# Performance work log

Measured on AMD Instinct MI355X. Metric: run time of the kernel, lower is better.

The kernel has to match this reference:

```python
import jax, jax.numpy as jnp
import numpy as np

N_NODES = 100000
N_EDGES = 1600000
DIMS = [21, 32, 64, 128, 21]  # conv1..conv4 (conv4 in-dim fixed to 128; source's 100 is a bug)


def _glorot(key, fan_in, fan_out):
    s = jnp.sqrt(6.0 / (fan_in + fan_out))
    return jax.random.uniform(key, (fan_in, fan_out), jnp.float32, -s, s)


def setup_inputs() -> dict:
    key = jax.random.key(0)
    ks = jax.random.split(key, 6)
    x = jax.random.normal(ks[0], (N_NODES, DIMS[0]), jnp.float32)
    edge_index = jax.random.randint(ks[1], (2, N_EDGES), 0, N_NODES, jnp.int64)
    inp = {"x": x, "edge_index": edge_index}
    wkeys = jax.random.split(ks[2], 4)
    for i in range(4):
        inp[f"W{i+1}"] = _glorot(wkeys[i], DIMS[i], DIMS[i + 1])
        inp[f"b{i+1}"] = jnp.zeros((DIMS[i + 1],), jnp.float32)
    return inp


def gcn_conv(x, row, col, W, b):
    # PyG GCNConv: h = x W; symmetric normalization with self loops; aggregate; + bias
    N = x.shape[0]
    h = x @ W  # [N, F]
    deg = jnp.zeros((N,), h.dtype).at[col].add(1.0) + 1.0  # +1 for self loop
    dinv = jax.lax.rsqrt(deg)
    norm = dinv[row] * dinv[col]  # [E]
    agg = jnp.zeros_like(h).at[col].add(norm[:, None] * h[row])  # scatter messages
    agg = agg + (dinv * dinv)[:, None] * h  # self-loop contribution
    return agg + b


def reference(x, edge_index, W1, b1, W2, b2, W3, b3, W4, b4):
    row, col = edge_index[0], edge_index[1]
    x = jax.nn.relu(gcn_conv(x, row, col, W1, b1))
    x = jax.nn.relu(gcn_conv(x, row, col, W2, b2))
    x = jax.nn.relu(gcn_conv(x, row, col, W3, b3))
    x = gcn_conv(x, row, col, W4, b4)
    return x
```

## Files before the change

### kernel.cpp

```cpp
#include <hip/hip_runtime.h>

#define NN 100000
#define NE 1600000
#define SH 7
#define NB_BKT 782
#define BCAP 3072
#define CSRCAP 3200
#define CHUNK 8192

static inline int cdiv(long long a, int b) { return (int)((a + b - 1) / b); }

__global__ void partition_kernel(const int* __restrict__ row, const int* __restrict__ col,
                                 int* __restrict__ bcur,
                                 unsigned int* __restrict__ packed, int E) {
    __shared__ int lh[NB_BKT];
    __shared__ int lbase[NB_BKT];
    for (int i = threadIdx.x; i < NB_BKT; i += 256) lh[i] = 0;
    __syncthreads();
    int base = blockIdx.x * CHUNK;
    int end = min(base + CHUNK, E);
    for (int e = base + threadIdx.x; e < end; e += 256) atomicAdd(&lh[col[e] >> SH], 1);
    __syncthreads();
    for (int i = threadIdx.x; i < NB_BKT; i += 256) {
        int v = lh[i];
        lbase[i] = v ? atomicAdd(&bcur[i], v) : 0;
        lh[i] = 0;
    }
    __syncthreads();
    for (int e = base + threadIdx.x; e < end; e += 256) {
        int c = col[e];
        int r = row[e];
        int b = c >> SH;
        int off = atomicAdd(&lh[b], 1);
        packed[lbase[b] + off] = ((unsigned)r << 7) | (unsigned)(c & 127);
    }
}

__global__ void bucket_nodes_place(const unsigned int* __restrict__ packed,
                                   const int* __restrict__ bcur, int* __restrict__ rowptr,
                                   int* __restrict__ rowend, float* __restrict__ dinv,
                                   int* __restrict__ csr_row, int N) {
    int b = blockIdx.x;
    __shared__ int lcnt[128];
    __shared__ int lcur[128];
    __shared__ int wt4[4];
    int t = threadIdx.x;
    if (t < 128) lcnt[t] = 0;
    __syncthreads();
    int s = b * BCAP;
    int e = bcur[b];
    for (int i = s + t; i < e; i += 256)
        atomicAdd(&lcnt[packed[i] & 127u], 1);
    __syncthreads();
    int node = (b << SH) + t;
    int v = (t < 128 && node < N) ? lcnt[t] + 1 : 0;
    int lane = t & 63, w = t >> 6;
    int incl = v;
#pragma unroll
    for (int off = 1; off < 64; off <<= 1) {
        int u = __shfl_up(incl, off, 64);
        if (lane >= off) incl += u;
    }
    if (lane == 63) wt4[w] = incl;
    __syncthreads();
    int woff = 0;
    for (int i = 0; i < w; i++) woff += wt4[i];
    int excl = woff + incl - v;
    if (t < 128 && node < N) {
        int start = b * CSRCAP + excl;
        rowptr[node] = start;
        rowend[node] = start + v;
        csr_row[start] = node;
        dinv[node] = rsqrtf((float)v);
        lcur[t] = start + 1;
    }
    __syncthreads();
    for (int i = s + t; i < e; i += 256) {
        unsigned p = packed[i];
        int r = (int)(p >> 7);
        int pos = atomicAdd(&lcur[p & 127u], 1);
        csr_row[pos] = r;
    }
}

__global__ void padx_kernel(const float* __restrict__ x, float* __restrict__ xp,
                            int* __restrict__ bcur, int N) {
    int idx = blockIdx.x * blockDim.x + threadIdx.x;
    if (idx < NB_BKT) bcur[idx] = idx * BCAP;
    if (idx >= N * 32) return;
    int n = idx >> 5;
    int k = idx & 31;
    xp[idx] = (k < 21) ? x[n * 21 + k] : 0.f;
}

template <int LPN, int FIN, int FOUT, int RJ, int OSTRIDE>
__global__ __launch_bounds__(512) void gather_gemm(
    const float4* __restrict__ h, const int* __restrict__ rowptr,
    const int* __restrict__ rowend, const int* __restrict__ csr_row,
    const float* __restrict__ dinv, const float* __restrict__ W,
    const float* __restrict__ b, float* __restrict__ out, int N) {
    constexpr int NT = 512 / LPN;
    constexpr int FINP = 4 * LPN;
    constexpr int XLD = FINP + 1;
    constexpr int JG = FOUT / RJ;
    __shared__ float xs[NT * XLD];
    __shared__ float Ws[FIN * FOUT];
    __shared__ float bs[FOUT];
    const int t = threadIdx.x;

    for (int i = t; i < FIN * FOUT; i += 512) Ws[i] = W[i];
    if (t < FOUT) bs[t] = b[t];

    const int l = t % LPN;
    const int ny = t / LPN;
    const int node = blockIdx.x * NT + ny;
    float4 acc = make_float4(0.f, 0.f, 0.f, 0.f);
    if (node < N) {
        int s = rowptr[node], e = rowend[node];
        float dn = dinv[node];
        int i = s;
        for (; i + 3 < e; i += 4) {
            int r0 = csr_row[i], r1 = csr_row[i + 1], r2 = csr_row[i + 2], r3 = csr_row[i + 3];
            float w0 = dinv[r0] * dn, w1 = dinv[r1] * dn, w2 = dinv[r2] * dn, w3 = dinv[r3] * dn;
            float4 a0 = h[(size_t)r0 * LPN + l];
            float4 a1 = h[(size_t)r1 * LPN + l];
            float4 a2 = h[(size_t)r2 * LPN + l];
            float4 a3 = h[(size_t)r3 * LPN + l];
            acc.x = fmaf(w0, a0.x, acc.x); acc.y = fmaf(w0, a0.y, acc.y);
            acc.z = fmaf(w0, a0.z, acc.z); acc.w = fmaf(w0, a0.w, acc.w);
            acc.x = fmaf(w1, a1.x, acc.x); acc.y = fmaf(w1, a1.y, acc.y);
            acc.z = fmaf(w1, a1.z, acc.z); acc.w = fmaf(w1, a1.w, acc.w);
            acc.x = fmaf(w2, a2.x, acc.x); acc.y = fmaf(w2, a2.y, acc.y);
            acc.z = fmaf(w2, a2.z, acc.z); acc.w = fmaf(w2, a2.w, acc.w);
            acc.x = fmaf(w3, a3.x, acc.x); acc.y = fmaf(w3, a3.y, acc.y);
            acc.z = fmaf(w3, a3.z, acc.z); acc.w = fmaf(w3, a3.w, acc.w);
        }
        for (; i < e; i++) {
            int r0 = csr_row[i];
            float w0 = dinv[r0] * dn;
            float4 a0 = h[(size_t)r0 * LPN + l];
            acc.x = fmaf(w0, a0.x, acc.x); acc.y = fmaf(w0, a0.y, acc.y);
            acc.z = fmaf(w0, a0.z, acc.z); acc.w = fmaf(w0, a0.w, acc.w);
        }
    }
    xs[ny * XLD + 4 * l + 0] = acc.x;
    xs[ny * XLD + 4 * l + 1] = acc.y;
    xs[ny * XLD + 4 * l + 2] = acc.z;
    xs[ny * XLD + 4 * l + 3] = acc.w;
    __syncthreads();

    const int jg = t % JG;
    const int ng = t / JG;
    float r[RJ];
#pragma unroll
    for (int jj = 0; jj < RJ; jj++) r[jj] = 0.f;
#pragma unroll 4
    for (int k = 0; k < FIN; k++) {
        float xv = xs[ng * XLD + k];
#pragma unroll
        for (int jj = 0; jj < RJ; jj++)
            r[jj] = fmaf(xv, Ws[k * FOUT + jg * RJ + jj], r[jj]);
    }
    int onode = blockIdx.x * NT + ng;
    if (onode < N) {
        float* orow = out + (size_t)onode * OSTRIDE + jg * RJ;
#pragma unroll
        for (int jj = 0; jj < RJ; jj++) r[jj] = fmaxf(r[jj] + bs[jg * RJ + jj], 0.f);
#pragma unroll
        for (int c = 0; c < RJ / 4; c++)
            *(float4*)&orow[4 * c] = make_float4(r[4 * c], r[4 * c + 1], r[4 * c + 2], r[4 * c + 3]);
    }
}

template <int LPN, bool BIAS, bool STORE21>
__global__ void gather4_kernel(const float4* __restrict__ h, const int* __restrict__ rowptr,
                               const int* __restrict__ rowend, const int* __restrict__ csr_row,
                               const float* __restrict__ dinv, const float* __restrict__ bias,
                               float* __restrict__ outp, int N) {
    int node = blockIdx.x * blockDim.y + threadIdx.y;
    if (node >= N) return;
    int l = threadIdx.x;
    int s = rowptr[node], e = rowend[node];
    float dn = dinv[node];
    float4 acc = make_float4(0.f, 0.f, 0.f, 0.f);
    int i = s;
    for (; i + 3 < e; i += 4) {
        int r0 = csr_row[i], r1 = csr_row[i + 1], r2 = csr_row[i + 2], r3 = csr_row[i + 3];
        float w0 = dinv[r0] * dn, w1 = dinv[r1] * dn, w2 = dinv[r2] * dn, w3 = dinv[r3] * dn;
        float4 a0 = h[(size_t)r0 * LPN + l];
        float4 a1 = h[(size_t)r1 * LPN + l];
        float4 a2 = h[(size_t)r2 * LPN + l];
        float4 a3 = h[(size_t)r3 * LPN + l];
        acc.x = fmaf(w0, a0.x, acc.x); acc.y = fmaf(w0, a0.y, acc.y);
        acc.z = fmaf(w0, a0.z, acc.z); acc.w = fmaf(w0, a0.w, acc.w);
        acc.x = fmaf(w1, a1.x, acc.x); acc.y = fmaf(w1, a1.y, acc.y);
        acc.z = fmaf(w1, a1.z, acc.z); acc.w = fmaf(w1, a1.w, acc.w);
        acc.x = fmaf(w2, a2.x, acc.x); acc.y = fmaf(w2, a2.y, acc.y);
        acc.z = fmaf(w2, a2.z, acc.z); acc.w = fmaf(w2, a2.w, acc.w);
        acc.x = fmaf(w3, a3.x, acc.x); acc.y = fmaf(w3, a3.y, acc.y);
        acc.z = fmaf(w3, a3.z, acc.z); acc.w = fmaf(w3, a3.w, acc.w);
    }
    for (; i < e; i++) {
        int r0 = csr_row[i];
        float w0 = dinv[r0] * dn;
        float4 a0 = h[(size_t)r0 * LPN + l];
        acc.x = fmaf(w0, a0.x, acc.x); acc.y = fmaf(w0, a0.y, acc.y);
        acc.z = fmaf(w0, a0.z, acc.z); acc.w = fmaf(w0, a0.w, acc.w);
    }
    if (STORE21) {
        int j = 4 * l;
        float v[4] = {acc.x, acc.y, acc.z, acc.w};
#pragma unroll
        for (int c = 0; c < 4; c++) {
            int jj = j + c;
            if (jj < 21) outp[(size_t)node * 21 + jj] = v[c] + (BIAS ? bias[jj] : 0.f);
        }
    } else {
        ((float4*)outp)[(size_t)node * LPN + l] = acc;
    }
}

__global__ __launch_bounds__(256, 3) void gemm_l3l4(
    const float* __restrict__ agg, const float* __restrict__ W3,
    const float* __restrict__ b3, const float* __restrict__ W4,
    float* __restrict__ out, int N) {
    __shared__ float4 W3v[64 * 32];
    __shared__ float4 W4v[16 * 48];
    __shared__ float b3s[128];
    const int t = threadIdx.x;
    const int node0 = blockIdx.x * 64;

    for (int sid = t; sid < 64 * 32; sid += 256) {
        int k = sid >> 5, q = sid & 31;
        int jg = q >> 2, c = q & 3;
        W3v[(k << 5) + (c << 3) + jg] = ((const float4*)W3)[sid];
    }
    for (int cid = t; cid < 16 * 48; cid += 256) {
        int i = cid / 48, rem = cid - i * 48;
        int jq = rem >> 3, jg = rem & 7;
        int k = jg * 16 + i;
        float v0 = (4 * jq + 0 < 21) ? W4[k * 21 + 4 * jq + 0] : 0.f;
        float v1 = (4 * jq + 1 < 21) ? W4[k * 21 + 4 * jq + 1] : 0.f;
        float v2 = (4 * jq + 2 < 21) ? W4[k * 21 + 4 * jq + 2] : 0.f;
        float v3 = (4 * jq + 3 < 21) ? W4[k * 21 + 4 * jq + 3] : 0.f;
        W4v[cid] = make_float4(v0, v1, v2, v3);
    }
    if (t < 128) b3s[t] = b3[t];
    __syncthreads();

    const int jg = t & 7;
    const int ng = t >> 3;
    const int nodeA = node0 + ng;
    const int nodeB = node0 + 32 + ng;
    const float* arowA = agg + (size_t)(nodeA < N ? nodeA : N - 1) * 64;
    const float* arowB = agg + (size_t)(nodeB < N ? nodeB : N - 1) * 64;

    float accA[16], accB[16];
#pragma unroll
    for (int jj = 0; jj < 16; jj++) { accA[jj] = 0.f; accB[jj] = 0.f; }
#pragma unroll 4
    for (int k = 0; k < 64; k++) {
        float xa = arowA[k];
        float xb = arowB[k];
        const float4* wb = &W3v[(k << 5) + jg];
#pragma unroll
        for (int c = 0; c < 4; c++) {
            float4 w = wb[c << 3];
            accA[4 * c + 0] = fmaf(xa, w.x, accA[4 * c + 0]);
            accA[4 * c + 1] = fmaf(xa, w.y, accA[4 * c + 1]);
            accA[4 * c + 2] = fmaf(xa, w.z, accA[4 * c + 2]);
            accA[4 * c + 3] = fmaf(xa, w.w, accA[4 * c + 3]);
            accB[4 * c + 0] = fmaf(xb, w.x, accB[4 * c + 0]);
            accB[4 * c + 1] = fmaf(xb, w.y, accB[4 * c + 1]);
            accB[4 * c + 2] = fmaf(xb, w.z, accB[4 * c + 2]);
            accB[4 * c + 3] = fmaf(xb, w.w, accB[4 * c + 3]);
        }
    }
#pragma unroll
    for (int jj = 0; jj < 16; jj++) {
        float bb = b3s[jg * 16 + jj];
        accA[jj] = fmaxf(accA[jj] + bb, 0.f);
        accB[jj] = fmaxf(accB[jj] + bb, 0.f);
    }

    float pA[24], pB[24];
#pragma unroll
    for (int j = 0; j < 24; j++) { pA[j] = 0.f; pB[j] = 0.f; }
#pragma unroll
    for (int i = 0; i < 16; i++) {
        float ha = accA[i];
        float hb = accB[i];
        const float4* wb = &W4v[i * 48 + jg];
#pragma unroll
        for (int jq = 0; jq < 6; jq++) {
            float4 w = wb[jq << 3];
            pA[4 * jq + 0] = fmaf(ha, w.x, pA[4 * jq + 0]);
            pA[4 * jq + 1] = fmaf(ha, w.y, pA[4 * jq + 1]);
            pA[4 * jq + 2] = fmaf(ha, w.z, pA[4 * jq + 2]);
            pA[4 * jq + 3] = fmaf(ha, w.w, pA[4 * jq + 3]);
            pB[4 * jq + 0] = fmaf(hb, w.x, pB[4 * jq + 0]);
            pB[4 * jq + 1] = fmaf(hb, w.y, pB[4 * jq + 1]);
            pB[4 * jq + 2] = fmaf(hb, w.z, pB[4 * jq + 2]);
            pB[4 * jq + 3] = fmaf(hb, w.w, pB[4 * jq + 3]);
        }
    }
#pragma unroll
    for (int m = 1; m < 8; m <<= 1) {
#pragma unroll
        for (int j = 0; j < 24; j++) {
            pA[j] += __shfl_xor(pA[j], m, 8);
            pB[j] += __shfl_xor(pB[j], m, 8);
        }
    }
    if (nodeA < N) {
        float* orow = out + (size_t)nodeA * 32 + jg * 3;
        orow[0] = pA[jg * 3 + 0];
        orow[1] = pA[jg * 3 + 1];
        orow[2] = pA[jg * 3 + 2];
        if (jg < 2) *(float4*)(out + (size_t)nodeA * 32 + 24 + 4 * jg) =
            make_float4(0.f, 0.f, 0.f, 0.f);
    }
    if (nodeB < N) {
        float* orow = out + (size_t)nodeB * 32 + jg * 3;
        orow[0] = pB[jg * 3 + 0];
        orow[1] = pB[jg * 3 + 1];
        orow[2] = pB[jg * 3 + 2];
        if (jg < 2) *(float4*)(out + (size_t)nodeB * 32 + 24 + 4 * jg) =
            make_float4(0.f, 0.f, 0.f, 0.f);
    }
}

extern "C" void kernel_launch(void* const* d_in, const int* in_sizes, int n_in,
                              void* d_out, int out_size, void* d_ws, size_t ws_size,
                              hipStream_t stream) {
    const float* x  = (const float*)d_in[0];
    const int*   ei = (const int*)d_in[1];
    const float* W1 = (const float*)d_in[2]; const float* b1 = (const float*)d_in[3];
    const float* W2 = (const float*)d_in[4]; const float* b2 = (const float*)d_in[5];
    const float* W3 = (const float*)d_in[6]; const float* b3 = (const float*)d_in[7];
    const float* W4 = (const float*)d_in[8]; const float* b4 = (const float*)d_in[9];
    const int* row = ei;
    const int* col = ei + NE;
    float* out = (float*)d_out;

    float* A      = (float*)d_ws;
    float* B      = A + (size_t)NN * 128;
    float* dinv   = B + (size_t)NN * 128;
    int*   rowptr = (int*)(dinv + NN);
    int*   rowend = rowptr + NN;
    int*   csr_row= rowend + NN;
    int*   bcur   = csr_row + (size_t)NB_BKT * CSRCAP;
    unsigned int* packed = (unsigned int*)A;

    const int BS = 256;
    const int NCH = cdiv(NE, CHUNK);

    padx_kernel<<<cdiv((long long)NN * 32, BS), BS, 0, stream>>>(x, B, bcur, NN);
    partition_kernel<<<NCH, 256, 0, stream>>>(row, col, bcur, packed, NE);
    bucket_nodes_place<<<NB_BKT, 256, 0, stream>>>(packed, bcur, rowptr, rowend, dinv, csr_row, NN);

    gather_gemm<8, 21, 32, 4, 32><<<cdiv(NN, 64), 512, 0, stream>>>(
        (const float4*)B, rowptr, rowend, csr_row, dinv, W1, b1, A, NN);
    gather_gemm<8, 32, 64, 8, 64><<<cdiv(NN, 64), 512, 0, stream>>>(
        (const float4*)A, rowptr, rowend, csr_row, dinv, W2, b2, B, NN);
    {
        dim3 blk(16, 16);
        gather4_kernel<16, false, false><<<cdiv(NN, 16), blk, 0, stream>>>(
            (const float4*)B, rowptr, rowend, csr_row, dinv, nullptr, A, NN);
    }
    gemm_l3l4<<<cdiv(NN, 64), 256, 0, stream>>>(A, W3, b3, W4, B, NN);
    {
        dim3 blk(8, 32);
        gather4_kernel<8, true, true><<<cdiv(NN, 32), blk, 0, stream>>>(
            (const float4*)B, rowptr, rowend, csr_row, dinv, b4, out, NN);
    }
}
```

Baseline: 337.4 us.

## Fuse layer-3 neighbor gather into the L3/L4 GEMM kernel via shared memory

Replaces the separate 64-wide gather kernel and the L3/L4 GEMM kernel with a single kernel. Each block first aggregates neighbor features for 64 nodes into an LDS tile, then runs the W3 and W4 products from shared memory. This removes the global write and re-read of the aggregated intermediate and one kernel launch. In exchange, blocks grow to 512 threads with more LDS, and each thread computes one node rather than two, which may reduce per-thread reuse of the weights.

```diff
diff --git a/kernel.cpp b/kernel.cpp
--- a/kernel.cpp
+++ b/kernel.cpp
@@ -220,22 +220,25 @@
     }
 }
 
-__global__ __launch_bounds__(256, 3) void gemm_l3l4(
-    const float* __restrict__ agg, const float* __restrict__ W3,
+__global__ __launch_bounds__(512, 4) void gather_gemm_l3l4(
+    const float4* __restrict__ h, const int* __restrict__ rowptr,
+    const int* __restrict__ rowend, const int* __restrict__ csr_row,
+    const float* __restrict__ dinv, const float* __restrict__ W3,
     const float* __restrict__ b3, const float* __restrict__ W4,
     float* __restrict__ out, int N) {
+    __shared__ float xs[64 * 65];
     __shared__ float4 W3v[64 * 32];
     __shared__ float4 W4v[16 * 48];
     __shared__ float b3s[128];
     const int t = threadIdx.x;
     const int node0 = blockIdx.x * 64;
 
-    for (int sid = t; sid < 64 * 32; sid += 256) {
+    for (int sid = t; sid < 64 * 32; sid += 512) {
         int k = sid >> 5, q = sid & 31;
         int jg = q >> 2, c = q & 3;
         W3v[(k << 5) + (c << 3) + jg] = ((const float4*)W3)[sid];
     }
-    for (int cid = t; cid < 16 * 48; cid += 256) {
+    for (int cid = t; cid < 16 * 48; cid += 512) {
         int i = cid / 48, rem = cid - i * 48;
         int jq = rem >> 3, jg = rem & 7;
         int k = jg * 16 + i;
@@ -246,22 +249,75 @@
         W4v[cid] = make_float4(v0, v1, v2, v3);
     }
     if (t < 128) b3s[t] = b3[t];
+
+    {
+        const int l = t & 7;
+        const int ny = t >> 3;
+        const int node = node0 + ny;
+        float4 acc0 = make_float4(0.f, 0.f, 0.f, 0.f);
+        float4 acc1 = make_float4(0.f, 0.f, 0.f, 0.f);
+        if (node < N) {
+            int s = rowptr[node], e = rowend[node];
+            float dn = dinv[node];
+            int i = s;
+            for (; i + 3 < e; i += 4) {
+                int r0 = csr_row[i], r1 = csr_row[i + 1];
+                int r2 = csr_row[i + 2], r3 = csr_row[i + 3];
+                float w0 = dinv[r0] * dn, w1 = dinv[r1] * dn;
+                float w2 = dinv[r2] * dn, w3 = dinv[r3] * dn;
+                const float4* p0 = h + (size_t)r0 * 16 + 2 * l;
+                const float4* p1 = h + (size_t)r1 * 16 + 2 * l;
+                const float4* p2 = h + (size_t)r2 * 16 + 2 * l;
+                const float4* p3 = h + (size_t)r3 * 16 + 2 * l;
+                float4 a0 = p0[0], c0 = p0[1];
+                float4 a1 = p1[0], c1 = p1[1];
+                float4 a2 = p2[0], c2 = p2[1];
+                float4 a3 = p3[0], c3 = p3[1];
+                acc0.x = fmaf(w0, a0.x, acc0.x); acc0.y = fmaf(w0, a0.y, acc0.y);
+                acc0.z = fmaf(w0, a0.z, acc0.z); acc0.w = fmaf(w0, a0.w, acc0.w);
+                acc1.x = fmaf(w0, c0.x, acc1.x); acc1.y = fmaf(w0, c0.y, acc1.y);
+                acc1.z = fmaf(w0, c0.z, acc1.z); acc1.w = fmaf(w0, c0.w, acc1.w);
+                acc0.x = fmaf(w1, a1.x, acc0.x); acc0.y = fmaf(w1, a1.y, acc0.y);
+                acc0.z = fmaf(w1, a1.z, acc0.z); acc0.w = fmaf(w1, a1.w, acc0.w);
+                acc1.x = fmaf(w1, c1.x, acc1.x); acc1.y = fmaf(w1, c1.y, acc1.y);
+                acc1.z = fmaf(w1, c1.z, acc1.z); acc1.w = fmaf(w1, c1.w, acc1.w);
+                acc0.x = fmaf(w2, a2.x, acc0.x); acc0.y = fmaf(w2, a2.y, acc0.y);
+                acc0.z = fmaf(w2, a2.z, acc0.z); acc0.w = fmaf(w2, a2.w, acc0.w);
+                acc1.x = fmaf(w2, c2.x, acc1.x); acc1.y = fmaf(w2, c2.y, acc1.y);
+                acc1.z = fmaf(w2, c2.z, acc1.z); acc1.w = fmaf(w2, c2.w, acc1.w);
+                acc0.x = fmaf(w3, a3.x, acc0.x); acc0.y = fmaf(w3, a3.y, acc0.y);
+                acc0.z = fmaf(w3, a3.z, acc0.z); acc0.w = fmaf(w3, a3.w, acc0.w);
+                acc1.x = fmaf(w3, c3.x, acc1.x); acc1.y = fmaf(w3, c3.y, acc1.y);
+                acc1.z = fmaf(w3, c3.z, acc1.z); acc1.w = fmaf(w3, c3.w, acc1.w);
+            }
+            for (; i < e; i++) {
+                int r0 = csr_row[i];
+                float w0 = dinv[r0] * dn;
+                const float4* p0 = h + (size_t)r0 * 16 + 2 * l;
+                float4 a0 = p0[0], c0 = p0[1];
+                acc0.x = fmaf(w0, a0.x, acc0.x); acc0.y = fmaf(w0, a0.y, acc0.y);
+                acc0.z = fmaf(w0, a0.z, acc0.z); acc0.w = fmaf(w0, a0.w, acc0.w);
+                acc1.x = fmaf(w0, c0.x, acc1.x); acc1.y = fmaf(w0, c0.y, acc1.y);
+                acc1.z = fmaf(w0, c0.z, acc1.z); acc1.w = fmaf(w0, c0.w, acc1.w);
+            }
+        }
+        float* xr = xs + ny * 65 + 8 * l;
+        xr[0] = acc0.x; xr[1] = acc0.y; xr[2] = acc0.z; xr[3] = acc0.w;
+        xr[4] = acc1.x; xr[5] = acc1.y; xr[6] = acc1.z; xr[7] = acc1.w;
+    }
     __syncthreads();
 
     const int jg = t & 7;
     const int ng = t >> 3;
-    const int nodeA = node0 + ng;
-    const int nodeB = node0 + 32 + ng;
-    const float* arowA = agg + (size_t)(nodeA < N ? nodeA : N - 1) * 64;
-    const float* arowB = agg + (size_t)(nodeB < N ? nodeB : N - 1) * 64;
-
-    float accA[16], accB[16];
-#pragma unroll
-    for (int jj = 0; jj < 16; jj++) { accA[jj] = 0.f; accB[jj] = 0.f; }
+    const int node = node0 + ng;
+    const float* arow = xs + ng * 65;
+
+    float accA[16];
+#pragma unroll
+    for (int jj = 0; jj < 16; jj++) accA[jj] = 0.f;
 #pragma unroll 4
     for (int k = 0; k < 64; k++) {
-        float xa = arowA[k];
-        float xb = arowB[k];
+        float xa = arow[k];
         const float4* wb = &W3v[(k << 5) + jg];
 #pragma unroll
         for (int c = 0; c < 4; c++) {
@@ -270,26 +326,20 @@
             accA[4 * c + 1] = fmaf(xa, w.y, accA[4 * c + 1]);
             accA[4 * c + 2] = fmaf(xa, w.z, accA[4 * c + 2]);
             accA[4 * c + 3] = fmaf(xa, w.w, accA[4 * c + 3]);
-            accB[4 * c + 0] = fmaf(xb, w.x, accB[4 * c + 0]);
-            accB[4 * c + 1] = fmaf(xb, w.y, accB[4 * c + 1]);
-            accB[4 * c + 2] = fmaf(xb, w.z, accB[4 * c + 2]);
-            accB[4 * c + 3] = fmaf(xb, w.w, accB[4 * c + 3]);
         }
     }
 #pragma unroll
     for (int jj = 0; jj < 16; jj++) {
         float bb = b3s[jg * 16 + jj];
         accA[jj] = fmaxf(accA[jj] + bb, 0.f);
-        accB[jj] = fmaxf(accB[jj] + bb, 0.f);
-    }
-
-    float pA[24], pB[24];
-#pragma unroll
-    for (int j = 0; j < 24; j++) { pA[j] = 0.f; pB[j] = 0.f; }
+    }
+
+    float pA[24];
+#pragma unroll
+    for (int j = 0; j < 24; j++) pA[j] = 0.f;
 #pragma unroll
     for (int i = 0; i < 16; i++) {
         float ha = accA[i];
-        float hb = accB[i];
         const float4* wb = &W4v[i * 48 + jg];
 #pragma unroll
         for (int jq = 0; jq < 6; jq++) {
@@ -298,34 +348,20 @@
             pA[4 * jq + 1] = fmaf(ha, w.y, pA[4 * jq + 1]);
             pA[4 * jq + 2] = fmaf(ha, w.z, pA[4 * jq + 2]);
             pA[4 * jq + 3] = fmaf(ha, w.w, pA[4 * jq + 3]);
-            pB[4 * jq + 0] = fmaf(hb, w.x, pB[4 * jq + 0]);
-            pB[4 * jq + 1] = fmaf(hb, w.y, pB[4 * jq + 1]);
-            pB[4 * jq + 2] = fmaf(hb, w.z, pB[4 * jq + 2]);
-            pB[4 * jq + 3] = fmaf(hb, w.w, pB[4 * jq + 3]);
         }
     }
 #pragma unroll
     for (int m = 1; m < 8; m <<= 1) {
 #pragma unroll
-        for (int j = 0; j < 24; j++) {
+        for (int j = 0; j < 24; j++)
             pA[j] += __shfl_xor(pA[j], m, 8);
-            pB[j] += __shfl_xor(pB[j], m, 8);
-        }
-    }
-    if (nodeA < N) {
-        float* orow = out + (size_t)nodeA * 32 + jg * 3;
+    }
+    if (node < N) {
+        float* orow = out + (size_t)node * 32 + jg * 3;
         orow[0] = pA[jg * 3 + 0];
         orow[1] = pA[jg * 3 + 1];
         orow[2] = pA[jg * 3 + 2];
-        if (jg < 2) *(float4*)(out + (size_t)nodeA * 32 + 24 + 4 * jg) =
-            make_float4(0.f, 0.f, 0.f, 0.f);
-    }
-    if (nodeB < N) {
-        float* orow = out + (size_t)nodeB * 32 + jg * 3;
-        orow[0] = pB[jg * 3 + 0];
-        orow[1] = pB[jg * 3 + 1];
-        orow[2] = pB[jg * 3 + 2];
-        if (jg < 2) *(float4*)(out + (size_t)nodeB * 32 + 24 + 4 * jg) =
+        if (jg < 2) *(float4*)(out + (size_t)node * 32 + 24 + 4 * jg) =
             make_float4(0.f, 0.f, 0.f, 0.f);
     }
 }
@@ -363,15 +399,11 @@
         (const float4*)B, rowptr, rowend, csr_row, dinv, W1, b1, A, NN);
     gather_gemm<8, 32, 64, 8, 64><<<cdiv(NN, 64), 512, 0, stream>>>(
         (const float4*)A, rowptr, rowend, csr_row, dinv, W2, b2, B, NN);
-    {
-        dim3 blk(16, 16);
-        gather4_kernel<16, false, false><<<cdiv(NN, 16), blk, 0, stream>>>(
-            (const float4*)B, rowptr, rowend, csr_row, dinv, nullptr, A, NN);
-    }
-    gemm_l3l4<<<cdiv(NN, 64), 256, 0, stream>>>(A, W3, b3, W4, B, NN);
+    gather_gemm_l3l4<<<cdiv(NN, 64), 512, 0, stream>>>(
+        (const float4*)B, rowptr, rowend, csr_row, dinv, W3, b3, W4, A, NN);
     {
         dim3 blk(8, 32);
         gather4_kernel<8, true, true><<<cdiv(NN, 32), blk, 0, stream>>>(
-            (const float4*)B, rowptr, rowend, csr_row, dinv, b4, out, NN);
-    }
-}
+            (const float4*)A, rowptr, rowend, csr_row, dinv, b4, out, NN);
+    }
+}
```

New measurement: 330.8 us. No clear change (-2.0%).
